# Optimization experiments

Measured on AMD Instinct MI355X. Metric: run time of the kernel, lower is better.

The kernel has to match this reference:

```python
import jax, jax.numpy as jnp
import numpy as np
import math

B, N, H, D = 2, 2048, 16, 64
NUM_BUCKETS, MAX_DIST = 32, 128
MODEL = H * D


def _rel_pos_bucket(rel, num_buckets, max_distance):
    # T5-style bucketing (bidirectional): half the buckets for sign, half log-spaced.
    nb = num_buckets // 2
    ret = (rel >= 0).astype(jnp.int32) * nb
    n = jnp.abs(rel)
    max_exact = nb // 2
    is_small = n < max_exact
    n_safe = jnp.maximum(n, 1).astype(jnp.float32)
    val_large = max_exact + (
        jnp.log(n_safe / max_exact) / math.log(max_distance / max_exact) * (nb - max_exact)
    ).astype(jnp.int32)
    val_large = jnp.minimum(val_large, nb - 1)
    return ret + jnp.where(is_small, n, val_large)


def _rel_pos_bias(rel_emb, n, m):
    q_pos = jnp.arange(m - n, m)
    k_pos = jnp.arange(m)
    rel = k_pos[None, :] - q_pos[:, None]            # [n, m]
    buckets = _rel_pos_bucket(rel, NUM_BUCKETS, MAX_DIST)
    bias = rel_emb[buckets]                          # [n, m, h]
    return bias.transpose(2, 0, 1)[None]             # [1, h, n, m]


def setup_inputs() -> dict:
    key = jax.random.key(0)
    ks = jax.random.split(key, 6)
    return {
        "q": jax.random.normal(ks[0], (B, N, MODEL), dtype=jnp.float32),
        "k": jax.random.normal(ks[1], (B, N, MODEL), dtype=jnp.float32),
        "v": jax.random.normal(ks[2], (B, N, MODEL), dtype=jnp.float32),
        "rel_emb": jax.random.normal(ks[3], (NUM_BUCKETS, H), dtype=jnp.float32) * 0.05,
        "w_out": jax.random.normal(ks[4], (MODEL, MODEL), dtype=jnp.float32) * (MODEL ** -0.5),
        "b_out": jax.random.normal(ks[5], (MODEL,), dtype=jnp.float32) * 0.02,
    }


def reference(q, k, v, rel_emb, w_out, b_out):
    b, n, _ = q.shape
    split = lambda x: x.reshape(b, n, H, D).transpose(0, 2, 1, 3)  # b h n d
    qh, kh, vh = split(q), split(k), split(v)
    sim = jnp.einsum('bhnd,bhmd->bhnm', qh, kh)
    sim = (sim + _rel_pos_bias(rel_emb, n, n)) * (D ** -0.5)  # note: scale AFTER bias, as in source
    attn = jax.nn.softmax(sim, axis=-1)
    out = jnp.einsum('bhnm,bhmd->bhnd', attn, vh)
    out = out.transpose(0, 2, 1, 3).reshape(b, n, H * D)
    return out @ w_out.T + b_out
```

## Files before the change

kernel.cpp:

```cpp
#include <hip/hip_runtime.h>

#define BB 2
#define NN 2048
#define HH 16
#define MODEL 1024
#define CSC 0.18033688011112042f

typedef short bf16x8 __attribute__((ext_vector_type(8)));
typedef float f32x4 __attribute__((ext_vector_type(4)));

__device__ __forceinline__ unsigned short f2bf(float x) {
  unsigned int u = __builtin_bit_cast(unsigned int, x);
  u += 0x7fffu + ((u >> 16) & 1u);
  return (unsigned short)(u >> 16);
}

__device__ __forceinline__ unsigned int pack_bf2(float a, float b) {
  unsigned int ua = __builtin_bit_cast(unsigned int, a) + 0x8000u;
  unsigned int ub = __builtin_bit_cast(unsigned int, b) + 0x8000u;
  return __builtin_amdgcn_perm(ub, ua, 0x07060302u);
}

__device__ __forceinline__ float fast_exp2(float x) {
#if __has_builtin(__builtin_amdgcn_exp2f)
  return __builtin_amdgcn_exp2f(x);
#else
  return exp2f(x);
#endif
}

__device__ __forceinline__ f32x4 mfma16(bf16x8 a, bf16x8 b, f32x4 c) {
  return __builtin_amdgcn_mfma_f32_16x16x32_bf16(a, b, c, 0, 0, 0);
}

__device__ __forceinline__ void async_copy16(void* lds_base, const void* g) {
  __builtin_amdgcn_global_load_lds(
      (const __attribute__((address_space(1))) void*)g,
      (__attribute__((address_space(3))) void*)lds_base, 16, 0, 0);
}

__global__ void cvt_kernel(const float* __restrict__ src,
                           unsigned short* __restrict__ dst, int n4) {
  int i = blockIdx.x * blockDim.x + threadIdx.x;
  if (i < n4) {
    float4 f = reinterpret_cast<const float4*>(src)[i];
    ushort4 u;
    u.x = f2bf(f.x); u.y = f2bf(f.y); u.z = f2bf(f.z); u.w = f2bf(f.w);
    reinterpret_cast<ushort4*>(dst)[i] = u;
  }
}

__global__ void transpose_v_kernel(const float* __restrict__ v,
                                   unsigned short* __restrict__ vt) {
  __shared__ unsigned short tile[64][65];
  int n0 = blockIdx.x * 64;
  int bh = blockIdx.y;
  int b = bh >> 4, h = bh & 15;
  int c = threadIdx.x & 63;
  int r = threadIdx.x >> 6;
#pragma unroll
  for (int i = 0; i < 16; ++i) {
    int nl = r * 16 + i;
    tile[c][nl] = f2bf(v[((long)(b * NN + n0 + nl)) * MODEL + h * 64 + c]);
  }
  __syncthreads();
#pragma unroll
  for (int i = 0; i < 16; ++i) {
    int d = r * 16 + i;
    vt[((long)(bh * 64 + d)) * NN + n0 + c] = tile[d][c];
  }
}

__global__ void bias_table_kernel(const float* __restrict__ rel_emb,
                                  float* __restrict__ biasTab) {
  int idx = blockIdx.x * 256 + threadIdx.x;
  if (idx >= 4095) return;
  int rel = idx - 2047;
  int nn = rel < 0 ? -rel : rel;
  int bucket;
  if (nn < 8) {
    bucket = nn;
  } else {
    float val = logf((float)nn * 0.125f) / logf(16.0f) * 8.0f;
    int vl = 8 + (int)val;
    if (vl > 15) vl = 15;
    bucket = vl;
  }
  if (rel >= 0) bucket += 16;
#pragma unroll
  for (int h = 0; h < 16; ++h)
    biasTab[h * 4095 + idx] = rel_emb[bucket * 16 + h] * CSC;
}

__global__ __launch_bounds__(256, 2) void flash2(
    const unsigned short* __restrict__ qb, const unsigned short* __restrict__ kb,
    const unsigned short* __restrict__ vtb, const float* __restrict__ biasTab,
    unsigned short* __restrict__ attn) {
  __shared__ __align__(16) float obuf[4 * 64 * 68];
  __shared__ __align__(16) float scratch[512];

  const int qt = blockIdx.x, bh = blockIdx.y;
  const int b = bh >> 4, h = bh & 15;
  const int q0 = qt * 64;
  const int tid = threadIdx.x, w = tid >> 6, lane = tid & 63;
  const int g = lane >> 4, c = lane & 15;

  const float* btab = biasTab + h * 4095 + 2047;
  for (int i = tid; i < 441; i += 256) scratch[i] = btab[i - 220];
  const float cPos = btab[200], cNeg = btab[-200];
  __syncthreads();

  bf16x8 qf0[4], qf1[4];
  const unsigned short* qbase = qb + ((long)(b * NN + q0)) * MODEL + h * 64;
#pragma unroll
  for (int nt = 0; nt < 4; ++nt) {
    const unsigned short* r = qbase + (16 * nt + c) * MODEL + 8 * g;
    qf0[nt] = *reinterpret_cast<const bf16x8*>(r);
    qf1[nt] = *reinterpret_cast<const bf16x8*>(r + 32);
  }

  const unsigned short* kbase = kb + ((long)b * NN) * MODEL + h * 64;
  const unsigned short* vbase = vtb + ((long)bh * 64) * NN;

  f32x4 o[4][4];
  float m_i[4], l_i[4];
#pragma unroll
  for (int nt = 0; nt < 4; ++nt) {
    m_i[nt] = -1e30f; l_i[nt] = 0.f;
#pragma unroll
    for (int mt = 0; mt < 4; ++mt) o[mt][nt] = f32x4{0.f, 0.f, 0.f, 0.f};
  }

  unsigned int* Pb = reinterpret_cast<unsigned int*>(obuf);
  const int ProwW = (w * 16 + c) * 36 + 2 * g;
  const int ProwR = (w * 16 + c) * 36 + 4 * g;

  for (int it = 0; it < 8; ++it) {
    const int kt = w + 4 * it;
    bf16x8 kf0[4], kf1[4];
    const unsigned short* krow = kbase + (long)(kt * 64) * MODEL;
#pragma unroll
    for (int mt = 0; mt < 4; ++mt) {
      const unsigned short* r = krow + (16 * mt + c) * MODEL + 8 * g;
      kf0[mt] = *reinterpret_cast<const bf16x8*>(r);
      kf1[mt] = *reinterpret_cast<const bf16x8*>(r + 32);
    }
    f32x4 s[4][4];
#pragma unroll
    for (int mt = 0; mt < 4; ++mt)
#pragma unroll
      for (int nt = 0; nt < 4; ++nt) {
        s[mt][nt] = mfma16(kf0[mt], qf0[nt], f32x4{0.f, 0.f, 0.f, 0.f});
        s[mt][nt] = mfma16(kf1[mt], qf1[nt], s[mt][nt]);
      }
    bf16x8 vf0[4], vf1[4];
    const unsigned short* vrow = vbase + kt * 64;
#pragma unroll
    for (int mt = 0; mt < 4; ++mt) {
      const unsigned short* r = vrow + (long)(16 * mt + c) * NN + 8 * g;
      vf0[mt] = *reinterpret_cast<const bf16x8*>(r);
      vf1[mt] = *reinterpret_cast<const bf16x8*>(r + 32);
    }
    const int lo = kt * 64 - q0 - 63, hi = kt * 64 + 63 - q0;
    if (lo >= 91 || hi <= -91) {
      const float cb = (lo >= 91) ? cPos : cNeg;
#pragma unroll
      for (int mt = 0; mt < 4; ++mt)
#pragma unroll
        for (int nt = 0; nt < 4; ++nt)
#pragma unroll
          for (int rr = 0; rr < 4; ++rr)
            s[mt][nt][rr] = s[mt][nt][rr] * CSC + cb;
    } else {
      const int base = kt * 64 + 4 * g - q0 - c + 220;
#pragma unroll
      for (int mt = 0; mt < 4; ++mt)
#pragma unroll
        for (int nt = 0; nt < 4; ++nt) {
          const int idx = base + 16 * mt - 16 * nt;
#pragma unroll
          for (int rr = 0; rr < 4; ++rr)
            s[mt][nt][rr] = s[mt][nt][rr] * CSC + scratch[idx + rr];
        }
    }
#pragma unroll
    for (int nt = 0; nt < 4; ++nt) {
      float mx = s[0][nt][0];
#pragma unroll
      for (int mt = 0; mt < 4; ++mt)
#pragma unroll
        for (int rr = 0; rr < 4; ++rr) mx = fmaxf(mx, s[mt][nt][rr]);
      mx = fmaxf(mx, __shfl_xor(mx, 16));
      mx = fmaxf(mx, __shfl_xor(mx, 32));
      const float mn = fmaxf(m_i[nt], mx);
      const float al = fast_exp2(m_i[nt] - mn);
      m_i[nt] = mn;
      float sum = 0.f;
      unsigned int pk[4][2];
#pragma unroll
      for (int mt = 0; mt < 4; ++mt)
#pragma unroll
        for (int t = 0; t < 2; ++t) {
          const float p0 = fast_exp2(s[mt][nt][2 * t] - mn);
          const float p1 = fast_exp2(s[mt][nt][2 * t + 1] - mn);
          sum += p0 + p1;
          pk[mt][t] = pack_bf2(p0, p1);
        }
      sum += __shfl_xor(sum, 16);
      sum += __shfl_xor(sum, 32);
      l_i[nt] = l_i[nt] * al + sum;
#pragma unroll
      for (int mt = 0; mt < 4; ++mt) {
        o[mt][nt][0] *= al; o[mt][nt][1] *= al;
        o[mt][nt][2] *= al; o[mt][nt][3] *= al;
      }
#pragma unroll
      for (int mt = 0; mt < 4; ++mt)
#pragma unroll
        for (int t = 0; t < 2; ++t)
          Pb[ProwW + 8 * mt + t] = pk[mt][t];
      const bf16x8 pb0 = *reinterpret_cast<const bf16x8*>(&Pb[ProwR]);
      const bf16x8 pb1 = *reinterpret_cast<const bf16x8*>(&Pb[ProwR + 16]);
#pragma unroll
      for (int mt = 0; mt < 4; ++mt) {
        o[mt][nt] = mfma16(vf0[mt], pb0, o[mt][nt]);
        o[mt][nt] = mfma16(vf1[mt], pb1, o[mt][nt]);
      }
    }
  }

  __syncthreads();
  float* ml = scratch;
  if (g == 0) {
#pragma unroll
    for (int nt = 0; nt < 4; ++nt) {
      ml[(w * 64 + 16 * nt + c) * 2] = m_i[nt];
      ml[(w * 64 + 16 * nt + c) * 2 + 1] = l_i[nt];
    }
  }
  float* ob = obuf + w * 64 * 68;
#pragma unroll
  for (int mt = 0; mt < 4; ++mt)
#pragma unroll
    for (int nt = 0; nt < 4; ++nt)
      *reinterpret_cast<f32x4*>(&ob[(16 * nt + c) * 68 + 16 * mt + 4 * g]) = o[mt][nt];
  __syncthreads();

  const int qr = 16 * w + c;
  float mu[4], lu[4];
#pragma unroll
  for (int u = 0; u < 4; ++u) {
    mu[u] = ml[(u * 64 + qr) * 2];
    lu[u] = ml[(u * 64 + qr) * 2 + 1];
  }
  float M = fmaxf(fmaxf(mu[0], mu[1]), fmaxf(mu[2], mu[3]));
  float L = 0.f, fu[4];
#pragma unroll
  for (int u = 0; u < 4; ++u) {
    fu[u] = fast_exp2(mu[u] - M);
    L += fu[u] * lu[u];
  }
  const float inv = 1.f / L;
  float acc[16];
#pragma unroll
  for (int j = 0; j < 16; ++j) acc[j] = 0.f;
#pragma unroll
  for (int u = 0; u < 4; ++u) {
    const float* src = obuf + u * 64 * 68 + qr * 68;
    f32x4 r0 = *reinterpret_cast<const f32x4*>(&src[8 * g]);
    f32x4 r1 = *reinterpret_cast<const f32x4*>(&src[8 * g + 4]);
    f32x4 r2 = *reinterpret_cast<const f32x4*>(&src[32 + 8 * g]);
    f32x4 r3 = *reinterpret_cast<const f32x4*>(&src[32 + 8 * g + 4]);
#pragma unroll
    for (int j = 0; j < 4; ++j) {
      acc[j] += fu[u] * r0[j];
      acc[4 + j] += fu[u] * r1[j];
      acc[8 + j] += fu[u] * r2[j];
      acc[12 + j] += fu[u] * r3[j];
    }
  }
  unsigned int od[8];
#pragma unroll
  for (int t = 0; t < 8; ++t) od[t] = pack_bf2(acc[2 * t] * inv, acc[2 * t + 1] * inv);
  unsigned short* orow = attn + ((long)(b * NN + q0 + qr)) * MODEL + h * 64;
  *reinterpret_cast<uint4*>(orow + 8 * g) = uint4{od[0], od[1], od[2], od[3]};
  *reinterpret_cast<uint4*>(orow + 32 + 8 * g) = uint4{od[4], od[5], od[6], od[7]};
}

__global__ void proj_gemm_kernel(const unsigned short* __restrict__ A,
                                 const unsigned short* __restrict__ Bw,
                                 const float* __restrict__ bias,
                                 float* __restrict__ out) {
  __shared__ __align__(16) unsigned short At[128 * 32];
  __shared__ __align__(16) unsigned short Bt[64 * 32];
  int bm0 = blockIdx.x * 128, bn0 = blockIdx.y * 64;
  int tid = threadIdx.x, w = tid >> 6, lane = tid & 63;
  int g = lane >> 4, c = lane & 15;
  int m0 = (w & 1) * 64, n0 = (w >> 1) * 32;

  f32x4 zero = {0.f, 0.f, 0.f, 0.f};
  f32x4 acc[4][2];
#pragma unroll
  for (int mi = 0; mi < 4; ++mi)
#pragma unroll
    for (int nj = 0; nj < 2; ++nj) acc[mi][nj] = zero;

  int rl4 = lane >> 2, p4 = lane & 3;
  for (int kt = 0; kt < 32; ++kt) {
    __syncthreads();
#pragma unroll
    for (int t = 0; t < 2; ++t) {
      int row = w * 32 + t * 16 + rl4;
      int lc = p4 ^ (rl4 & 3);
      async_copy16(&At[(w * 32 + t * 16) * 32],
                   A + (long)(bm0 + row) * 1024 + kt * 32 + lc * 8);
    }
    {
      int row = w * 16 + rl4;
      int lc = p4 ^ (rl4 & 3);
      async_copy16(&Bt[(w * 16) * 32],
                   Bw + (long)(bn0 + row) * 1024 + kt * 32 + lc * 8);
    }
    __syncthreads();

    bf16x8 af[4], bfr[2];
#pragma unroll
    for (int mi = 0; mi < 4; ++mi) {
      int row = m0 + mi * 16 + c;
      af[mi] = *reinterpret_cast<const bf16x8*>(&At[row * 32 + (g ^ (row & 3)) * 8]);
    }
#pragma unroll
    for (int nj = 0; nj < 2; ++nj) {
      int row = n0 + nj * 16 + c;
      bfr[nj] = *reinterpret_cast<const bf16x8*>(&Bt[row * 32 + (g ^ (row & 3)) * 8]);
    }
#pragma unroll
    for (int mi = 0; mi < 4; ++mi)
#pragma unroll
      for (int nj = 0; nj < 2; ++nj)
        acc[mi][nj] = mfma16(af[mi], bfr[nj], acc[mi][nj]);
  }

#pragma unroll
  for (int mi = 0; mi < 4; ++mi)
#pragma unroll
    for (int nj = 0; nj < 2; ++nj)
#pragma unroll
      for (int r = 0; r < 4; ++r) {
        int row = bm0 + m0 + mi * 16 + 4 * g + r;
        int col = bn0 + n0 + nj * 16 + c;
        out[(long)row * 1024 + col] = acc[mi][nj][r] + bias[col];
      }
}

extern "C" void kernel_launch(void* const* d_in, const int* in_sizes, int n_in,
                              void* d_out, int out_size, void* d_ws, size_t ws_size,
                              hipStream_t stream) {
  const float* q = (const float*)d_in[0];
  const float* k = (const float*)d_in[1];
  const float* v = (const float*)d_in[2];
  const float* rel_emb = (const float*)d_in[3];
  const float* w_out = (const float*)d_in[4];
  const float* b_out = (const float*)d_in[5];
  float* out = (float*)d_out;

  char* ws = (char*)d_ws;
  unsigned short* qb   = (unsigned short*)(ws);
  unsigned short* kb   = (unsigned short*)(ws + (8u << 20));
  unsigned short* vt   = (unsigned short*)(ws + (16u << 20));
  unsigned short* attn = (unsigned short*)(ws + (24u << 20));
  unsigned short* wb   = (unsigned short*)(ws + (32u << 20));
  float* biasTab       = (float*)(ws + (34u << 20));

  hipLaunchKernelGGL(cvt_kernel, dim3(4096), dim3(256), 0, stream,
                     q, qb, BB * NN * MODEL / 4);
  hipLaunchKernelGGL(cvt_kernel, dim3(4096), dim3(256), 0, stream,
                     k, kb, BB * NN * MODEL / 4);
  hipLaunchKernelGGL(cvt_kernel, dim3(1024), dim3(256), 0, stream,
                     w_out, wb, MODEL * MODEL / 4);
  hipLaunchKernelGGL(transpose_v_kernel, dim3(NN / 64, BB * HH), dim3(256), 0, stream,
                     v, vt);
  hipLaunchKernelGGL(bias_table_kernel, dim3(16), dim3(256), 0, stream,
                     rel_emb, biasTab);
  hipLaunchKernelGGL(flash2, dim3(NN / 64, BB * HH), dim3(256), 0, stream,
                     qb, kb, vt, biasTab, attn);
  hipLaunchKernelGGL(proj_gemm_kernel, dim3(32, 16), dim3(256), 0, stream,
                     attn, wb, b_out, out);
}
```

Baseline: 224.6 us.

## Halve flash epilogue LDS, raise occupancy bound, fuse conversion kernels

Three separate fp32-to-bf16 conversion launches are merged into one kernel that picks its source by index range. The flash kernel's output-merge buffer is halved by staging the accumulator in two passes with extra barriers, and launch bounds are raised to 4 blocks per CU. The P tile is now written to LDS with a vector store. The aim is higher flash-attention occupancy and fewer launches, at the cost of more register pressure (possible spills) and extra synchronization in the epilogue.

```diff
diff --git a/kernel.cpp b/kernel.cpp
--- a/kernel.cpp
+++ b/kernel.cpp
@@ -39,15 +39,28 @@
       (__attribute__((address_space(3))) void*)lds_base, 16, 0, 0);
 }
 
-__global__ void cvt_kernel(const float* __restrict__ src,
-                           unsigned short* __restrict__ dst, int n4) {
-  int i = blockIdx.x * blockDim.x + threadIdx.x;
-  if (i < n4) {
-    float4 f = reinterpret_cast<const float4*>(src)[i];
-    ushort4 u;
-    u.x = f2bf(f.x); u.y = f2bf(f.y); u.z = f2bf(f.z); u.w = f2bf(f.w);
-    reinterpret_cast<ushort4*>(dst)[i] = u;
-  }
+__global__ void cvt3_kernel(const float* __restrict__ q, const float* __restrict__ k,
+                            const float* __restrict__ w, unsigned short* __restrict__ qb,
+                            unsigned short* __restrict__ kb, unsigned short* __restrict__ wb) {
+  const int NQ = BB * NN * MODEL / 4;
+  const int NW = MODEL * MODEL / 4;
+  int i = blockIdx.x * 256 + threadIdx.x;
+  const float* src;
+  unsigned short* dst;
+  int j = i;
+  if (i < NQ) {
+    src = q; dst = qb;
+  } else if (i < 2 * NQ) {
+    src = k; dst = kb; j = i - NQ;
+  } else if (i < 2 * NQ + NW) {
+    src = w; dst = wb; j = i - 2 * NQ;
+  } else {
+    return;
+  }
+  float4 f = reinterpret_cast<const float4*>(src)[j];
+  ushort4 u;
+  u.x = f2bf(f.x); u.y = f2bf(f.y); u.z = f2bf(f.z); u.w = f2bf(f.w);
+  reinterpret_cast<ushort4*>(dst)[j] = u;
 }
 
 __global__ void transpose_v_kernel(const float* __restrict__ v,
@@ -92,11 +105,11 @@
     biasTab[h * 4095 + idx] = rel_emb[bucket * 16 + h] * CSC;
 }
 
-__global__ __launch_bounds__(256, 2) void flash2(
+__global__ __launch_bounds__(256, 4) void flash3(
     const unsigned short* __restrict__ qb, const unsigned short* __restrict__ kb,
     const unsigned short* __restrict__ vtb, const float* __restrict__ biasTab,
     unsigned short* __restrict__ attn) {
-  __shared__ __align__(16) float obuf[4 * 64 * 68];
+  __shared__ __align__(16) float obuf[4 * 64 * 36];
   __shared__ __align__(16) float scratch[512];
 
   const int qt = blockIdx.x, bh = blockIdx.y;
@@ -216,9 +229,7 @@
       }
 #pragma unroll
       for (int mt = 0; mt < 4; ++mt)
-#pragma unroll
-        for (int t = 0; t < 2; ++t)
-          Pb[ProwW + 8 * mt + t] = pk[mt][t];
+        *reinterpret_cast<uint2*>(&Pb[ProwW + 8 * mt]) = uint2{pk[mt][0], pk[mt][1]};
       const bf16x8 pb0 = *reinterpret_cast<const bf16x8*>(&Pb[ProwR]);
       const bf16x8 pb1 = *reinterpret_cast<const bf16x8*>(&Pb[ProwR + 16]);
 #pragma unroll
@@ -238,12 +249,12 @@
       ml[(w * 64 + 16 * nt + c) * 2 + 1] = l_i[nt];
     }
   }
-  float* ob = obuf + w * 64 * 68;
-#pragma unroll
-  for (int mt = 0; mt < 4; ++mt)
+#pragma unroll
+  for (int mt = 0; mt < 2; ++mt)
 #pragma unroll
     for (int nt = 0; nt < 4; ++nt)
-      *reinterpret_cast<f32x4*>(&ob[(16 * nt + c) * 68 + 16 * mt + 4 * g]) = o[mt][nt];
+      *reinterpret_cast<f32x4*>(
+          &obuf[(w * 64 + 16 * nt + c) * 36 + 16 * mt + 4 * g]) = o[mt][nt];
   __syncthreads();
 
   const int qr = 16 * w + c;
@@ -261,24 +272,42 @@
     L += fu[u] * lu[u];
   }
   const float inv = 1.f / L;
+
   float acc[16];
 #pragma unroll
   for (int j = 0; j < 16; ++j) acc[j] = 0.f;
 #pragma unroll
   for (int u = 0; u < 4; ++u) {
-    const float* src = obuf + u * 64 * 68 + qr * 68;
+    const float* src = obuf + (u * 64 + qr) * 36;
     f32x4 r0 = *reinterpret_cast<const f32x4*>(&src[8 * g]);
     f32x4 r1 = *reinterpret_cast<const f32x4*>(&src[8 * g + 4]);
-    f32x4 r2 = *reinterpret_cast<const f32x4*>(&src[32 + 8 * g]);
-    f32x4 r3 = *reinterpret_cast<const f32x4*>(&src[32 + 8 * g + 4]);
 #pragma unroll
     for (int j = 0; j < 4; ++j) {
       acc[j] += fu[u] * r0[j];
       acc[4 + j] += fu[u] * r1[j];
-      acc[8 + j] += fu[u] * r2[j];
-      acc[12 + j] += fu[u] * r3[j];
-    }
-  }
+    }
+  }
+  __syncthreads();
+
+#pragma unroll
+  for (int mt = 2; mt < 4; ++mt)
+#pragma unroll
+    for (int nt = 0; nt < 4; ++nt)
+      *reinterpret_cast<f32x4*>(
+          &obuf[(w * 64 + 16 * nt + c) * 36 + 16 * (mt - 2) + 4 * g]) = o[mt][nt];
+  __syncthreads();
+#pragma unroll
+  for (int u = 0; u < 4; ++u) {
+    const float* src = obuf + (u * 64 + qr) * 36;
+    f32x4 r0 = *reinterpret_cast<const f32x4*>(&src[8 * g]);
+    f32x4 r1 = *reinterpret_cast<const f32x4*>(&src[8 * g + 4]);
+#pragma unroll
+    for (int j = 0; j < 4; ++j) {
+      acc[8 + j] += fu[u] * r0[j];
+      acc[12 + j] += fu[u] * r1[j];
+    }
+  }
+
   unsigned int od[8];
 #pragma unroll
   for (int t = 0; t < 8; ++t) od[t] = pack_bf2(acc[2 * t] * inv, acc[2 * t + 1] * inv);
@@ -372,17 +401,13 @@
   unsigned short* wb   = (unsigned short*)(ws + (32u << 20));
   float* biasTab       = (float*)(ws + (34u << 20));
 
-  hipLaunchKernelGGL(cvt_kernel, dim3(4096), dim3(256), 0, stream,
-                     q, qb, BB * NN * MODEL / 4);
-  hipLaunchKernelGGL(cvt_kernel, dim3(4096), dim3(256), 0, stream,
-                     k, kb, BB * NN * MODEL / 4);
-  hipLaunchKernelGGL(cvt_kernel, dim3(1024), dim3(256), 0, stream,
-                     w_out, wb, MODEL * MODEL / 4);
+  hipLaunchKernelGGL(cvt3_kernel, dim3(9216), dim3(256), 0, stream,
+                     q, k, w_out, qb, kb, wb);
   hipLaunchKernelGGL(transpose_v_kernel, dim3(NN / 64, BB * HH), dim3(256), 0, stream,
                      v, vt);
   hipLaunchKernelGGL(bias_table_kernel, dim3(16), dim3(256), 0, stream,
                      rel_emb, biasTab);
-  hipLaunchKernelGGL(flash2, dim3(NN / 64, BB * HH), dim3(256), 0, stream,
+  hipLaunchKernelGGL(flash3, dim3(NN / 64, BB * HH), dim3(256), 0, stream,
                      qb, kb, vt, biasTab, attn);
   hipLaunchKernelGGL(proj_gemm_kernel, dim3(32, 16), dim3(256), 0, stream,
                      attn, wb, b_out, out);
```

Measured after the change: 528.8 us. +135.5%, slower.
